# Kernel optimization log

Hardware: AMD Instinct MI355X
Metric: run time of the kernel (lower is better)

## Reference

```python
import jax, jax.numpy as jnp
import numpy as np

ITERS = 5          # iter_node_counts
N, M, Z, E = 68, 46, 384, 368   # base VNs, base CNs, lifting size, total base edges
LLR_CLIP = 20.0    # allowed_llr_range.abs
BIG = 1e9


def setup_inputs() -> dict:
    key = jax.random.key(0)
    k1, k2, k3 = jax.random.split(key, 3)
    B = 64
    # channel LLRs, realistic AWGN-ish magnitudes
    xa = jax.random.normal(k1, (B, N, Z), dtype=jnp.float32) * 4.0
    edge_vn = jax.random.randint(k2, (E,), 0, N, dtype=jnp.int32)
    # regular check degree 8 so every check has >=2 edges (valid min-sum extrinsics)
    edge_cn = (jnp.arange(E, dtype=jnp.int32) % M)
    edge_shift = jax.random.randint(k3, (E,), 0, Z, dtype=jnp.int32)  # circulant shifts
    cn_weight = jnp.ones((ITERS,), dtype=jnp.float32)  # scalar CN weight per iteration
    return {"xa": xa, "cn_weight": cn_weight, "edge_vn": edge_vn,
            "edge_cn": edge_cn, "edge_shift": edge_shift}


def _qms5(x):
    # QMS q_bit=5 quantizer with straight-through estimator
    q = jnp.clip(jnp.round(x * 2.0) / 2.0, -7.5, 7.5)
    xc = jnp.clip(x, -7.5, 7.5)
    return xc + jax.lax.stop_gradient(q - xc)


def _decode(xa, cn_weight, edge_vn, edge_cn, edge_shift):
    B = xa.shape[0]
    xa_in = jnp.transpose(xa, (0, 2, 1))  # [B, Z, N]
    z = jnp.arange(Z)
    # lifting (Lift_Matrix1): cyclic shift each edge's Z copies; unlift is inverse
    idx_lift = ((z[:, None] - edge_shift[None, :]) % Z)[None]    # [1, Z, E]
    idx_unlift = ((z[:, None] + edge_shift[None, :]) % Z)[None]  # [1, Z, E]
    c2v = jnp.zeros((B, Z, E), dtype=xa.dtype)  # prev_llr (CN->VN messages)
    ch = jnp.moveaxis(xa_in, 2, 0)  # [N, B, Z]
    outs = []
    for it in range(ITERS):
        # --- odd layer (VN update): W_skipconn2even + W_odd2even ---
        vn_sum = jax.ops.segment_sum(jnp.moveaxis(c2v, 2, 0), edge_vn, num_segments=N)  # [N,B,Z]
        tot = ch + vn_sum                                  # total belief per VN
        v2c = jnp.moveaxis(tot[edge_vn], 0, 2) - c2v       # extrinsic, [B,Z,E]
        v2c = jnp.clip(v2c, -LLR_CLIP, LLR_CLIP)           # allowed_llr_range
        v2c = jnp.take_along_axis(v2c, idx_lift, axis=1)   # Lift_Matrix1
        # --- even layer (CN update, min-sum): W_even2odd ---
        vE = jnp.moveaxis(v2c, 2, 0)                       # [E, B, Z]
        mag = jnp.abs(vE)
        neg = (vE < 0).astype(jnp.int32)
        cnt = jax.ops.segment_sum(neg, edge_cn, num_segments=M)      # [M,B,Z]
        csign = (1 - 2 * (cnt % 2)).astype(vE.dtype)                 # sign product per CN
        min1 = jax.ops.segment_min(mag, edge_cn, num_segments=M)
        is_min = mag == min1[edge_cn]
        min2 = jax.ops.segment_min(jnp.where(is_min, BIG, mag), edge_cn, num_segments=M)
        ext_min = jnp.where(is_min, min2[edge_cn], min1[edge_cn])
        own_sign = jnp.where(vE < 0, -1.0, 1.0).astype(vE.dtype)
        ext = csign[edge_cn] * own_sign * ext_min          # extrinsic min-sum message
        ext = _qms5(cn_weight[it] * ext)                   # learned CN weight + QMS quantize
        c2v = jnp.moveaxis(ext, 0, 2)                      # [B,Z,E]
        c2v = jnp.take_along_axis(c2v, idx_unlift, axis=1) # Lift_Matrix2
        # --- output marginalization: W_output ---
        out = xa_in + jnp.moveaxis(
            jax.ops.segment_sum(jnp.moveaxis(c2v, 2, 0), edge_vn, num_segments=N), 0, 2)
        outs.append(out)
    return jnp.stack(outs)  # [ITERS, B, Z, N]


def reference(xa, cn_weight, edge_vn, edge_cn, edge_shift):
    return _decode(xa, cn_weight, edge_vn, edge_cn, edge_shift)
```

## Files before the change

kernel.cpp:

```cpp
#include <hip/hip_runtime.h>


#define ITERS 5
#define Nn 68
#define Mm 46
#define Zz 384
#define Ee 368
#define Bb 64
#define Kk 8
#define PADD 24
#define BIGF 1e9f

#define ROWB (Bb*Zz)
#define TOT_ELEMS (Nn*Bb*Zz)
#define C2V_BYTES ((Ee+1)*ROWB)
#define TOT_OFF   0
#define C2V_OFF   (TOT_ELEMS*4)
#define BAR_OFF   (C2V_OFF + C2V_BYTES)

#define BLK 256
#define GBLK 24
#define GROUPS 64
#define CNU (Mm*Zz)
#define OUT_ITER ((size_t)Bb*Zz*Nn)

__device__ __forceinline__ void wait_vm0() {
    asm volatile("s_waitcnt vmcnt(0)" ::: "memory");
    __builtin_amdgcn_sched_barrier(0);
}
__device__ __forceinline__ void store_b8_llc(signed char* p, int q) {
    asm volatile("global_store_byte %0, %1, off sc0 sc1"
                 :: "v"(p), "v"(q) : "memory");
}
__device__ __forceinline__ void store_f32_llc(float* p, float s) {
    asm volatile("global_store_dword %0, %1, off sc0 sc1"
                 :: "v"(p), "v"(s) : "memory");
}

__device__ __forceinline__ void gbar(unsigned* __restrict__ ctr)
{
    __syncthreads();
    if (threadIdx.x == 0) {
        __hip_atomic_fetch_add(ctr, 1u, __ATOMIC_RELAXED,
                               __HIP_MEMORY_SCOPE_SYSTEM);
        int spins = 0;
        for (;;) {
            unsigned c = __hip_atomic_load(ctr, __ATOMIC_RELAXED,
                                           __HIP_MEMORY_SCOPE_SYSTEM);
            if (c >= (unsigned)GBLK) break;
            __builtin_amdgcn_s_sleep(4);
            if ((++spins & 31) == 0) {
                c = __hip_atomic_fetch_add(ctr, 0u, __ATOMIC_RELAXED,
                                           __HIP_MEMORY_SCOPE_SYSTEM);
                if (c >= (unsigned)GBLK) break;
            }
        }
    }
    __syncthreads();
}

__device__ __forceinline__ void minsum_store(
    const float v[Kk], const int off[Kk], float m1, unsigned sflip,
    float w, signed char* __restrict__ c2v)
{
    float m2 = BIGF;
    #pragma unroll
    for (int k = 0; k < Kk; k++) {
        float mag = fabsf(v[k]);
        if (mag != m1) m2 = fminf(m2, mag);
    }
    #pragma unroll
    for (int k = 0; k < Kk; k++) {
        float mag  = fabsf(v[k]);
        float emin = (mag == m1) ? m2 : m1;
        unsigned neg = sflip ^ ((v[k] < 0.0f) ? 1u : 0u);
        float ext = neg ? -emin : emin;
        float r = rintf(w * ext * 2.0f);
        r = fminf(15.0f, fmaxf(-15.0f, r));
        store_b8_llc(c2v + off[k], (int)r);
    }
}

template<bool FIRST>
__device__ __forceinline__ void cn_pass(
    const float* __restrict__ src,
    signed char* __restrict__ c2v,
    const int* __restrict__ edge_vn, const int* __restrict__ edge_shift,
    float w, int g, int r)
{
    for (int u = r * BLK + threadIdx.x; u < CNU; u += GBLK * BLK) {
        const int cn = __builtin_amdgcn_readfirstlane(u) / Zz;
        const int zc = u - cn * Zz;

        float v[Kk];
        int   off[Kk];
        float tv[Kk];
        int   cv[Kk];

        #pragma unroll
        for (int k = 0; k < Kk; k++) {
            int e  = cn + k * Mm;
            int sh = edge_shift[e];
            int n  = edge_vn[e];
            int z  = zc - sh;
            z += (z >> 31) & Zz;
            int o = e * ROWB + g * Zz + z;
            off[k] = o;
            if (FIRST) {
                tv[k] = src[(g * Nn + n) * Zz + z];
            } else {
                const float* tp = src + (n * Bb + g) * Zz + z;
                asm volatile("global_load_dword %0, %1, off sc0 sc1"
                             : "=v"(tv[k]) : "v"(tp));
                const signed char* cp = c2v + o;
                asm volatile("global_load_sbyte %0, %1, off sc0 sc1"
                             : "=v"(cv[k]) : "v"(cp));
            }
        }
        if (!FIRST) wait_vm0();

        float m1 = BIGF;
        unsigned sflip = 0u;
        #pragma unroll
        for (int k = 0; k < Kk; k++) {
            float x = FIRST ? tv[k]
                            : (tv[k] - 0.5f * (float)cv[k]);
            x = fminf(20.0f, fmaxf(-20.0f, x));
            v[k] = x;
            if (x < 0.0f) sflip ^= 1u;
            m1 = fminf(m1, fabsf(x));
        }
        minsum_store(v, off, m1, sflip, w, c2v);
    }
}

__device__ __forceinline__ void vn_pass(
    const float* __restrict__ xa, const signed char* __restrict__ c2v,
    float* __restrict__ tot, float* __restrict__ out_it,
    const int* __restrict__ sdeg, const int* __restrict__ svoff,
    int write_tot, float (*tile)[65], int g, int r)
{
    const int wave = threadIdx.x >> 6;
    const int lane = threadIdx.x & 63;
    const int zq = r >> 2, nc = r & 3;
    const int z0 = zq * 64, n0 = nc * 17;
    const int z  = z0 + lane;
    const int bz = g * Zz + z;

    for (int i = wave; i < 17; i += 4) {
        int n = __builtin_amdgcn_readfirstlane(n0 + i);
        int d = __builtin_amdgcn_readfirstlane(sdeg[n]);
        const int* vo = svoff + n * PADD;
        int q0[8], q1[8], q2[8];
        #pragma unroll
        for (int j = 0; j < 8; j++) {
            const signed char* p = c2v + (vo[j] + bz);
            asm volatile("global_load_sbyte %0, %1, off sc0 sc1"
                         : "=v"(q0[j]) : "v"(p));
        }
        if (d > 8) {
            #pragma unroll
            for (int j = 0; j < 8; j++) {
                const signed char* p = c2v + (vo[8 + j] + bz);
                asm volatile("global_load_sbyte %0, %1, off sc0 sc1"
                             : "=v"(q1[j]) : "v"(p));
            }
        }
        if (d > 16) {
            #pragma unroll
            for (int j = 0; j < 8; j++) {
                const signed char* p = c2v + (vo[16 + j] + bz);
                asm volatile("global_load_sbyte %0, %1, off sc0 sc1"
                             : "=v"(q2[j]) : "v"(p));
            }
        }
        wait_vm0();

        int acc = 0;
        #pragma unroll
        for (int j = 0; j < 8; j++) acc += q0[j];
        if (d > 8) {
            #pragma unroll
            for (int j = 0; j < 8; j++) acc += q1[j];
        }
        if (d > 16) {
            #pragma unroll
            for (int j = 0; j < 8; j++) acc += q2[j];
        }
        float s = xa[(size_t)(g * Nn + n) * Zz + z] + 0.5f * (float)acc;
        if (write_tot) store_f32_llc(tot + (n * Bb + g) * Zz + z, s);
        tile[i][lane] = s;
    }
    __syncthreads();

    float* dst = out_it + ((size_t)g * Zz + z0) * Nn + n0;
    for (int idx = threadIdx.x; idx < 17 * 64; idx += BLK) {
        int zz = idx / 17;
        int nn = idx - zz * 17;
        dst[(size_t)zz * Nn + nn] = tile[nn][zz];
    }
    __syncthreads();
}

__global__ __launch_bounds__(BLK, 6) void fused_kernel(
    const float* __restrict__ xa, const float* __restrict__ cn_weight,
    const int* __restrict__ edge_vn, const int* __restrict__ edge_shift,
    float* __restrict__ tot, signed char* __restrict__ c2v,
    unsigned* __restrict__ bar, float* __restrict__ out)
{
    __shared__ float tile[17][65];
    __shared__ int   svoff[Nn * PADD];
    __shared__ int   sdeg[Nn];

    const int r = blockIdx.x;
    const int g = blockIdx.y;

    for (int i = threadIdx.x; i < Nn; i += BLK) sdeg[i] = 0;
    for (int i = threadIdx.x; i < Nn * PADD; i += BLK) svoff[i] = Ee * ROWB;
    __syncthreads();
    for (int e = threadIdx.x; e < Ee; e += BLK) {
        int n = edge_vn[e];
        int slot = atomicAdd(&sdeg[n], 1);
        if (slot < PADD) svoff[n * PADD + slot] = e * ROWB;
    }
    if (r == 0) {
        int* p = (int*)(c2v + (size_t)Ee * ROWB + g * Zz);
        int zero = 0;
        for (int i = threadIdx.x; i < Zz / 4; i += BLK)
            asm volatile("global_store_dword %0, %1, off sc0 sc1"
                         :: "v"(p + i), "v"(zero) : "memory");
    }
    __syncthreads();

    unsigned* gb = bar + g * 16;

    for (int it = 0; it < ITERS; ++it) {
        const float w = cn_weight[it];
        if (it == 0) cn_pass<true >(xa,  c2v, edge_vn, edge_shift, w, g, r);
        else         cn_pass<false>(tot, c2v, edge_vn, edge_shift, w, g, r);
        gbar(gb + 2 * it);
        vn_pass(xa, c2v, tot, out + (size_t)it * OUT_ITER,
                sdeg, svoff, (it != ITERS - 1) ? 1 : 0, tile, g, r);
        if (it != ITERS - 1) gbar(gb + 2 * it + 1);
    }
}

extern "C" void kernel_launch(void* const* d_in, const int* in_sizes, int n_in,
                              void* d_out, int out_size, void* d_ws, size_t ws_size,
                              hipStream_t stream) {
    const float* xa        = (const float*)d_in[0];
    const float* cn_weight = (const float*)d_in[1];
    const int*   edge_vn   = (const int*)d_in[2];
    const int*   edge_shift= (const int*)d_in[4];
    float* out = (float*)d_out;

    char* ws = (char*)d_ws;
    float*       tot = (float*)(ws + TOT_OFF);
    signed char* c2v = (signed char*)(ws + C2V_OFF);
    unsigned*    bar = (unsigned*)(ws + BAR_OFF);

    hipMemsetAsync(ws + BAR_OFF, 0, GROUPS * 64, stream);

    fused_kernel<<<dim3(GBLK, GROUPS), dim3(BLK), 0, stream>>>(
        xa, cn_weight, edge_vn, edge_shift, tot, c2v, bar, out);
}
```

Baseline: 223.6 us.

## Software-pipeline CN and VN passes with compiler-visible LLC atomics

Replaces the inline-asm loads and stores, along with their explicit vmcnt(0) waits, with relaxed system-scope atomic loads and stores, so the compiler can schedule and overlap memory operations. The CN pass is unrolled into a fixed schedule of two or three work items per thread, issuing the next item's loads before consuming the previous one. The VN pass issues loads for all of a wave's rows up front before accumulating any of them. It also shortens the barrier sleep interval. The trade-offs are higher register pressure and reliance on the compiler to emit the same cache-coherent instructions.

Result: no change. 226.9 us (+1.5%).

```diff
diff --git a/kernel.cpp b/kernel.cpp
--- a/kernel.cpp
+++ b/kernel.cpp
@@ -22,19 +22,21 @@
 #define GBLK 24
 #define GROUPS 64
 #define CNU (Mm*Zz)
+#define STRIDE (GBLK*BLK)
 #define OUT_ITER ((size_t)Bb*Zz*Nn)
 
-__device__ __forceinline__ void wait_vm0() {
-    asm volatile("s_waitcnt vmcnt(0)" ::: "memory");
-    __builtin_amdgcn_sched_barrier(0);
-}
-__device__ __forceinline__ void store_b8_llc(signed char* p, int q) {
-    asm volatile("global_store_byte %0, %1, off sc0 sc1"
-                 :: "v"(p), "v"(q) : "memory");
-}
-__device__ __forceinline__ void store_f32_llc(float* p, float s) {
-    asm volatile("global_store_dword %0, %1, off sc0 sc1"
-                 :: "v"(p), "v"(s) : "memory");
+__device__ __forceinline__ float llc_ldf(const float* p) {
+    return __hip_atomic_load(p, __ATOMIC_RELAXED, __HIP_MEMORY_SCOPE_SYSTEM);
+}
+__device__ __forceinline__ int llc_ldb(const signed char* p) {
+    return (int)__hip_atomic_load(p, __ATOMIC_RELAXED, __HIP_MEMORY_SCOPE_SYSTEM);
+}
+__device__ __forceinline__ void llc_stb(signed char* p, int q) {
+    __hip_atomic_store(p, (signed char)q, __ATOMIC_RELAXED,
+                       __HIP_MEMORY_SCOPE_SYSTEM);
+}
+__device__ __forceinline__ void llc_stf(float* p, float v) {
+    __hip_atomic_store(p, v, __ATOMIC_RELAXED, __HIP_MEMORY_SCOPE_SYSTEM);
 }
 
 __device__ __forceinline__ void gbar(unsigned* __restrict__ ctr)
@@ -48,7 +50,7 @@
             unsigned c = __hip_atomic_load(ctr, __ATOMIC_RELAXED,
                                            __HIP_MEMORY_SCOPE_SYSTEM);
             if (c >= (unsigned)GBLK) break;
-            __builtin_amdgcn_s_sleep(4);
+            __builtin_amdgcn_s_sleep(2);
             if ((++spins & 31) == 0) {
                 c = __hip_atomic_fetch_add(ctr, 0u, __ATOMIC_RELAXED,
                                            __HIP_MEMORY_SCOPE_SYSTEM);
@@ -77,61 +79,127 @@
         float ext = neg ? -emin : emin;
         float r = rintf(w * ext * 2.0f);
         r = fminf(15.0f, fmaxf(-15.0f, r));
-        store_b8_llc(c2v + off[k], (int)r);
-    }
+        llc_stb(c2v + off[k], (int)r);
+    }
+}
+
+template<bool FIRST>
+__device__ __forceinline__ void cn_issue(
+    const float* __restrict__ src, const signed char* __restrict__ c2v,
+    const int* __restrict__ edge_vn, const int* __restrict__ edge_shift,
+    int g, int u, float tv[Kk], int cv[Kk], int off[Kk])
+{
+    const int cn = __builtin_amdgcn_readfirstlane(u) / Zz;
+    const int zc = u - cn * Zz;
+    #pragma unroll
+    for (int k = 0; k < Kk; k++) {
+        int e  = cn + k * Mm;
+        int sh = edge_shift[e];
+        int n  = edge_vn[e];
+        int z  = zc - sh;
+        z += (z >> 31) & Zz;
+        int o = e * ROWB + g * Zz + z;
+        off[k] = o;
+        if (FIRST) {
+            tv[k] = src[(g * Nn + n) * Zz + z];
+        } else {
+            tv[k] = llc_ldf(src + (n * Bb + g) * Zz + z);
+            cv[k] = llc_ldb(c2v + o);
+        }
+    }
+}
+
+template<bool FIRST>
+__device__ __forceinline__ void cn_consume(
+    float w, signed char* __restrict__ c2v,
+    const float tv[Kk], const int cv[Kk], const int off[Kk])
+{
+    float v[Kk];
+    float m1 = BIGF;
+    unsigned sflip = 0u;
+    #pragma unroll
+    for (int k = 0; k < Kk; k++) {
+        float x = FIRST ? tv[k]
+                        : (tv[k] - 0.5f * (float)cv[k]);
+        x = fminf(20.0f, fmaxf(-20.0f, x));
+        v[k] = x;
+        if (x < 0.0f) sflip ^= 1u;
+        m1 = fminf(m1, fabsf(x));
+    }
+    minsum_store(v, off, m1, sflip, w, c2v);
 }
 
 template<bool FIRST>
 __device__ __forceinline__ void cn_pass(
-    const float* __restrict__ src,
-    signed char* __restrict__ c2v,
+    const float* __restrict__ src, signed char* __restrict__ c2v,
     const int* __restrict__ edge_vn, const int* __restrict__ edge_shift,
     float w, int g, int r)
 {
-    for (int u = r * BLK + threadIdx.x; u < CNU; u += GBLK * BLK) {
-        const int cn = __builtin_amdgcn_readfirstlane(u) / Zz;
-        const int zc = u - cn * Zz;
-
-        float v[Kk];
-        int   off[Kk];
-        float tv[Kk];
-        int   cv[Kk];
-
+    const int start = r * BLK + (int)threadIdx.x;
+    float tv0[Kk], tv1[Kk], tv2[Kk];
+    int   cv0[Kk], cv1[Kk], cv2[Kk];
+    int   of0[Kk], of1[Kk], of2[Kk];
+    if (r < 21) {
+        cn_issue<FIRST>(src, c2v, edge_vn, edge_shift, g, start,            tv0, cv0, of0);
+        cn_issue<FIRST>(src, c2v, edge_vn, edge_shift, g, start + STRIDE,   tv1, cv1, of1);
+        cn_consume<FIRST>(w, c2v, tv0, cv0, of0);
+        cn_issue<FIRST>(src, c2v, edge_vn, edge_shift, g, start + 2*STRIDE, tv2, cv2, of2);
+        cn_consume<FIRST>(w, c2v, tv1, cv1, of1);
+        cn_consume<FIRST>(w, c2v, tv2, cv2, of2);
+    } else {
+        cn_issue<FIRST>(src, c2v, edge_vn, edge_shift, g, start,            tv0, cv0, of0);
+        cn_issue<FIRST>(src, c2v, edge_vn, edge_shift, g, start + STRIDE,   tv1, cv1, of1);
+        cn_consume<FIRST>(w, c2v, tv0, cv0, of0);
+        cn_consume<FIRST>(w, c2v, tv1, cv1, of1);
+    }
+}
+
+__device__ __forceinline__ void vn_issue_row(
+    const signed char* __restrict__ c2v, const float* __restrict__ xa,
+    const int* __restrict__ sdeg, const int* __restrict__ svoff,
+    int g, int z, int bz, int n0, int row,
+    int q[8], float* xv, int* dn, int* dd)
+{
+    int n = __builtin_amdgcn_readfirstlane(n0 + row);
+    int d = __builtin_amdgcn_readfirstlane(sdeg[n]);
+    const int* vo = svoff + n * PADD;
+    #pragma unroll
+    for (int j = 0; j < 8; j++) q[j] = llc_ldb(c2v + (vo[j] + bz));
+    *xv = xa[(size_t)(g * Nn + n) * Zz + z];
+    *dn = n; *dd = d;
+}
+
+__device__ __forceinline__ float vn_consume_row(
+    const signed char* __restrict__ c2v, const int* __restrict__ svoff,
+    int bz, int n, int d, const int q[8], float xv)
+{
+    int acc = 0;
+    if (d > 8) {
+        const int* vo = svoff + n * PADD;
+        int q1[8];
         #pragma unroll
-        for (int k = 0; k < Kk; k++) {
-            int e  = cn + k * Mm;
-            int sh = edge_shift[e];
-            int n  = edge_vn[e];
-            int z  = zc - sh;
-            z += (z >> 31) & Zz;
-            int o = e * ROWB + g * Zz + z;
-            off[k] = o;
-            if (FIRST) {
-                tv[k] = src[(g * Nn + n) * Zz + z];
-            } else {
-                const float* tp = src + (n * Bb + g) * Zz + z;
-                asm volatile("global_load_dword %0, %1, off sc0 sc1"
-                             : "=v"(tv[k]) : "v"(tp));
-                const signed char* cp = c2v + o;
-                asm volatile("global_load_sbyte %0, %1, off sc0 sc1"
-                             : "=v"(cv[k]) : "v"(cp));
-            }
+        for (int j = 0; j < 8; j++) q1[j] = llc_ldb(c2v + (vo[8 + j] + bz));
+        if (d > 16) {
+            int q2[8];
+            #pragma unroll
+            for (int j = 0; j < 8; j++) q2[j] = llc_ldb(c2v + (vo[16 + j] + bz));
+            #pragma unroll
+            for (int j = 0; j < 8; j++) acc += q[j];
+            #pragma unroll
+            for (int j = 0; j < 8; j++) acc += q1[j];
+            #pragma unroll
+            for (int j = 0; j < 8; j++) acc += q2[j];
+        } else {
+            #pragma unroll
+            for (int j = 0; j < 8; j++) acc += q[j];
+            #pragma unroll
+            for (int j = 0; j < 8; j++) acc += q1[j];
         }
-        if (!FIRST) wait_vm0();
-
-        float m1 = BIGF;
-        unsigned sflip = 0u;
+    } else {
         #pragma unroll
-        for (int k = 0; k < Kk; k++) {
-            float x = FIRST ? tv[k]
-                            : (tv[k] - 0.5f * (float)cv[k]);
-            x = fminf(20.0f, fmaxf(-20.0f, x));
-            v[k] = x;
-            if (x < 0.0f) sflip ^= 1u;
-            m1 = fminf(m1, fabsf(x));
-        }
-        minsum_store(v, off, m1, sflip, w, c2v);
-    }
+        for (int j = 0; j < 8; j++) acc += q[j];
+    }
+    return xv + 0.5f * (float)acc;
 }
 
 __device__ __forceinline__ void vn_pass(
@@ -147,49 +215,27 @@
     const int z  = z0 + lane;
     const int bz = g * Zz + z;
 
-    for (int i = wave; i < 17; i += 4) {
-        int n = __builtin_amdgcn_readfirstlane(n0 + i);
-        int d = __builtin_amdgcn_readfirstlane(sdeg[n]);
-        const int* vo = svoff + n * PADD;
-        int q0[8], q1[8], q2[8];
-        #pragma unroll
-        for (int j = 0; j < 8; j++) {
-            const signed char* p = c2v + (vo[j] + bz);
-            asm volatile("global_load_sbyte %0, %1, off sc0 sc1"
-                         : "=v"(q0[j]) : "v"(p));
-        }
-        if (d > 8) {
-            #pragma unroll
-            for (int j = 0; j < 8; j++) {
-                const signed char* p = c2v + (vo[8 + j] + bz);
-                asm volatile("global_load_sbyte %0, %1, off sc0 sc1"
-                             : "=v"(q1[j]) : "v"(p));
-            }
-        }
-        if (d > 16) {
-            #pragma unroll
-            for (int j = 0; j < 8; j++) {
-                const signed char* p = c2v + (vo[16 + j] + bz);
-                asm volatile("global_load_sbyte %0, %1, off sc0 sc1"
-                             : "=v"(q2[j]) : "v"(p));
-            }
-        }
-        wait_vm0();
-
-        int acc = 0;
-        #pragma unroll
-        for (int j = 0; j < 8; j++) acc += q0[j];
-        if (d > 8) {
-            #pragma unroll
-            for (int j = 0; j < 8; j++) acc += q1[j];
-        }
-        if (d > 16) {
-            #pragma unroll
-            for (int j = 0; j < 8; j++) acc += q2[j];
-        }
-        float s = xa[(size_t)(g * Nn + n) * Zz + z] + 0.5f * (float)acc;
-        if (write_tot) store_f32_llc(tot + (n * Bb + g) * Zz + z, s);
-        tile[i][lane] = s;
+    int q[4][8]; float xv[4]; int dn[4], dd[4];
+    #pragma unroll
+    for (int t = 0; t < 4; t++)
+        vn_issue_row(c2v, xa, sdeg, svoff, g, z, bz, n0, wave + 4 * t,
+                     q[t], &xv[t], &dn[t], &dd[t]);
+    int q4[8]; float xv4 = 0.0f; int dn4 = 0, dd4 = 0;
+    const bool has5 = (wave == 0);
+    if (has5)
+        vn_issue_row(c2v, xa, sdeg, svoff, g, z, bz, n0, 16,
+                     q4, &xv4, &dn4, &dd4);
+
+    #pragma unroll
+    for (int t = 0; t < 4; t++) {
+        float s = vn_consume_row(c2v, svoff, bz, dn[t], dd[t], q[t], xv[t]);
+        if (write_tot) llc_stf(tot + (dn[t] * Bb + g) * Zz + z, s);
+        tile[wave + 4 * t][lane] = s;
+    }
+    if (has5) {
+        float s = vn_consume_row(c2v, svoff, bz, dn4, dd4, q4, xv4);
+        if (write_tot) llc_stf(tot + (dn4 * Bb + g) * Zz + z, s);
+        tile[16][lane] = s;
     }
     __syncthreads();
 
@@ -225,10 +271,9 @@
     }
     if (r == 0) {
         int* p = (int*)(c2v + (size_t)Ee * ROWB + g * Zz);
-        int zero = 0;
         for (int i = threadIdx.x; i < Zz / 4; i += BLK)
-            asm volatile("global_store_dword %0, %1, off sc0 sc1"
-                         :: "v"(p + i), "v"(zero) : "memory");
+            __hip_atomic_store(p + i, 0, __ATOMIC_RELAXED,
+                               __HIP_MEMORY_SCOPE_SYSTEM);
     }
     __syncthreads();
 
```
